# Optimization experiments

Measured on AMD Instinct MI355X. Metric: run time of the kernel, lower is better.

Reference implementation:

```python
import jax, jax.numpy as jnp
import numpy as np

N, C, V, T = 16, 32, 512, 64
H, EMB, D = 4, 64, 16
OUT_C = 64
BN_EPS = 1e-5


def setup_inputs() -> dict:
    key = jax.random.key(0)
    ks = jax.random.split(key, 12)
    x = jax.random.normal(ks[0], (N, C, V, T), dtype=jnp.float32)
    t_in = jax.random.uniform(ks[1], (N, T), dtype=jnp.float32)
    # random-walk-like supports; scaled so chained nconv hops stay O(1)
    A0 = jax.random.normal(ks[2], (V, V), dtype=jnp.float32) * (V ** -0.5)
    A1 = jax.random.normal(ks[3], (V, V), dtype=jnp.float32) * (V ** -0.5)
    A2 = jax.random.normal(ks[4], (V, V), dtype=jnp.float32) * (V ** -0.5)
    factors = jax.random.normal(ks[5], (H,), dtype=jnp.float32) * 0.1
    Wq = jax.random.normal(ks[6], (H, EMB, D), dtype=jnp.float32) * (EMB ** -0.5)
    Wk = jax.random.normal(ks[7], (H, EMB, D), dtype=jnp.float32) * (EMB ** -0.5)
    GC_IN = 7 * C  # (order*support_len + 1) * in_channels
    W_out = jax.random.normal(ks[8], (OUT_C, GC_IN), dtype=jnp.float32) * (GC_IN ** -0.5)
    b_out = jnp.zeros((OUT_C,), dtype=jnp.float32)
    W_res = jax.random.normal(ks[9], (OUT_C, C), dtype=jnp.float32) * (C ** -0.5)
    b_res = jnp.zeros((OUT_C,), dtype=jnp.float32)
    bn_gamma = jnp.ones((OUT_C,), dtype=jnp.float32)
    bn_beta = jnp.zeros((OUT_C,), dtype=jnp.float32)
    bn_mean = jnp.zeros((OUT_C,), dtype=jnp.float32)
    bn_var = jnp.ones((OUT_C,), dtype=jnp.float32)
    alpha = jnp.full((1,), 0.25, dtype=jnp.float32)  # PReLU init
    return dict(x=x, t_in=t_in, A0=A0, A1=A1, A2=A2, factors=factors,
                Wq=Wq, Wk=Wk, W_out=W_out, b_out=b_out,
                W_res=W_res, b_res=b_res, bn_gamma=bn_gamma, bn_beta=bn_beta,
                bn_mean=bn_mean, bn_var=bn_var, alpha=alpha)


def reference(x, t_in, A0, A1, A2, factors, Wq, Wk, W_out, b_out,
              W_res, b_res, bn_gamma, bn_beta, bn_mean, bn_var, alpha):
    # --- learnEmbedding, all heads at once: emb[b,h,t,f] ---
    div = jnp.arange(0, EMB, 2, dtype=x.dtype)           # [EMB/2]
    div_term = jnp.exp(div[None, :] * factors[:, None])  # [H, EMB/2]
    phase = jnp.einsum('bt,hf->bhtf', t_in, div_term)    # [N,H,T,EMB/2]
    emb = jnp.concatenate([jnp.sin(phase), jnp.cos(phase)], axis=-1)  # [N,H,T,EMB]
    # --- ATT per head (t_out=None => q_emb == k_emb) ---
    q = jnp.einsum('bhtf,hfd->bhtd', emb, Wq)
    k = jnp.einsum('bhtf,hfd->bhtd', emb, Wk)
    att = jax.nn.softmax(jnp.einsum('bhtd,bhpd->bhtp', q, k) / (D ** 0.5), axis=-1)  # [N,H,T,T]
    # --- temporal mixing, summed over heads (matches per-head += loop) ---
    xt = jnp.einsum('ncvt,nhpt->ncvp', x, att)           # [N,C,V,T]
    # --- gcn: diffusion over 3 supports, order 2 ---
    outs = [xt]
    for A in (A0, A1, A2):
        x1 = jnp.einsum('ncvl,vw->ncwl', xt, A)
        x2 = jnp.einsum('ncvl,vw->ncwl', x1, A)
        outs.extend([x1, x2])
    h = jnp.concatenate(outs, axis=1)                    # [N,7C,V,T]
    # --- 1x1 output projection ---
    y = jnp.einsum('ncvt,oc->novt', h, W_out) + b_out[None, :, None, None]
    # --- residual branch: 1x1 conv + BatchNorm (eval) ---
    r = jnp.einsum('ncvt,oc->novt', x, W_res) + b_res[None, :, None, None]
    r = (r - bn_mean[None, :, None, None]) * jax.lax.rsqrt(bn_var + BN_EPS)[None, :, None, None]
    r = r * bn_gamma[None, :, None, None] + bn_beta[None, :, None, None]
    # --- residual add + PReLU (dropout is identity in eval) ---
    out = y + r
    out = jnp.where(out > 0, out, alpha[0] * out)
    return out
```

## Files before the change

kernel.cpp:

```cpp
#include <hip/hip_runtime.h>

namespace {
constexpr int N_ = 16, C_ = 32, V_ = 512, T_ = 64;
constexpr int H_ = 4, D_ = 16, OC_ = 64;
constexpr int EMB_ = 64;
constexpr int GCIN_ = 7 * C_;
constexpr int TV_ = T_ * V_;
}

typedef _Float16 f16x8 __attribute__((ext_vector_type(8)));
typedef _Float16 f16x4 __attribute__((ext_vector_type(4)));
typedef float f32x4 __attribute__((ext_vector_type(4)));

__global__ __launch_bounds__(64) void att_kernel(
    const float* __restrict__ t_in, const float* __restrict__ factors,
    const float* __restrict__ Wq, const float* __restrict__ Wk,
    float* __restrict__ att)
{
    const int n = blockIdx.x >> 2;
    const int h = blockIdx.x & 3;
    const int t = threadIdx.x;

    __shared__ float wq_l[EMB_][D_];
    __shared__ float wk_l[EMB_][D_];
    __shared__ float k_l[T_][D_ + 1];

#pragma unroll
    for (int d = 0; d < D_; ++d) {
        wq_l[t][d] = Wq[(h * EMB_ + t) * D_ + d];
        wk_l[t][d] = Wk[(h * EMB_ + t) * D_ + d];
    }
    __syncthreads();

    const float tv = t_in[n * T_ + t];
    const float fh = factors[h];
    float emb[EMB_];
#pragma unroll
    for (int j = 0; j < 32; ++j) {
        float dt = __expf((float)(2 * j) * fh);
        float ph = tv * dt;
        float s, c;
        __sincosf(ph, &s, &c);
        emb[j] = s;
        emb[j + 32] = c;
    }

    float q[D_];
#pragma unroll
    for (int d = 0; d < D_; ++d) {
        float aq = 0.f, ak = 0.f;
#pragma unroll
        for (int f = 0; f < EMB_; ++f) {
            aq += emb[f] * wq_l[f][d];
            ak += emb[f] * wk_l[f][d];
        }
        q[d] = aq;
        k_l[t][d] = ak;
    }
    __syncthreads();

    float L[T_];
    float m = -1e30f;
#pragma unroll
    for (int j = 0; j < T_; ++j) {
        float a = 0.f;
#pragma unroll
        for (int d = 0; d < D_; ++d) a += q[d] * k_l[j][d];
        a *= 0.25f;
        L[j] = a;
        m = fmaxf(m, a);
    }
    float ssum = 0.f;
#pragma unroll
    for (int j = 0; j < T_; ++j) {
        float e = __expf(L[j] - m);
        L[j] = e;
        ssum += e;
    }
    const float inv = 1.f / ssum;
    float* arow = att + (((size_t)(n * H_ + h) * T_ + t) * T_);
#pragma unroll
    for (int j = 0; j < T_; ++j) arow[j] = L[j] * inv;
}

__global__ __launch_bounds__(256) void sred_kernel(
    const float* __restrict__ att, float* __restrict__ S)
{
    int g = blockIdx.x * 256 + threadIdx.x;
    if (g >= N_ * T_ * T_) return;
    int n = g / (T_ * T_);
    int ij = g - n * (T_ * T_);
    float a = 0.f;
#pragma unroll
    for (int h = 0; h < H_; ++h) a += att[(size_t)(n * H_ + h) * (T_ * T_) + ij];
    S[g] = a;
}

__global__ __launch_bounds__(256) void prepAt_kernel(
    const float* __restrict__ A0, const float* __restrict__ A1,
    const float* __restrict__ A2, _Float16* __restrict__ At16)
{
    const int s = blockIdx.z;
    const float* A = (s == 0) ? A0 : ((s == 1) ? A1 : A2);
    const int v0 = blockIdx.y * 32, w0 = blockIdx.x * 32;
    const int tid = threadIdx.x;
    __shared__ float sT[32][33];
#pragma unroll
    for (int k = 0; k < 4; ++k) {
        int lin = k * 256 + tid;
        int i = lin >> 5, w = lin & 31;
        sT[i][w] = A[(size_t)(v0 + i) * V_ + w0 + w];
    }
    __syncthreads();
#pragma unroll
    for (int k = 0; k < 4; ++k) {
        int lin = k * 256 + tid;
        int j = lin >> 5, i = lin & 31;
        At16[(size_t)s * V_ * V_ + (size_t)(w0 + j) * V_ + v0 + i] = (_Float16)sT[i][j];
    }
}

__global__ __launch_bounds__(256) void prepxT_kernel(
    const float* __restrict__ x, _Float16* __restrict__ xT, int n0)
{
    const int b = blockIdx.z;
    const int v0 = blockIdx.x * 32;
    const int t0 = blockIdx.y * 32;
    const int tid = threadIdx.x;
    __shared__ float sT[32][33];
    const float* xb = x + ((size_t)(n0 * C_) + b) * (size_t)(V_ * T_);
    {
        int vi = tid >> 3, tq = tid & 7;
        *(float4*)&sT[vi][tq * 4] = *(const float4*)&xb[(size_t)(v0 + vi) * T_ + t0 + tq * 4];
    }
    __syncthreads();
    {
        int tj = tid >> 3, vq = tid & 7;
        f16x4 o4;
        o4[0] = (_Float16)sT[vq * 4 + 0][tj];
        o4[1] = (_Float16)sT[vq * 4 + 1][tj];
        o4[2] = (_Float16)sT[vq * 4 + 2][tj];
        o4[3] = (_Float16)sT[vq * 4 + 3][tj];
        *(f16x4*)&xT[(size_t)b * TV_ + (size_t)(t0 + tj) * V_ + v0 + vq * 4] = o4;
    }
}

__global__ __launch_bounds__(256) void prepW_kernel(
    const float* __restrict__ W_out, const float* __restrict__ b_out,
    const float* __restrict__ W_res, const float* __restrict__ b_res,
    const float* __restrict__ gamma, const float* __restrict__ beta,
    const float* __restrict__ mean, const float* __restrict__ var,
    _Float16* __restrict__ Wcat, float* __restrict__ bias)
{
    const int tid = threadIdx.x;
    const int o = tid & 63;
    const int kb = tid >> 6;
    const float rs = gamma[o] * rsqrtf(var[o] + 1e-5f);
    for (int kk = 0; kk < 64; ++kk) {
        int k = kb * 64 + kk;
        float w = (k < GCIN_) ? W_out[o * GCIN_ + k] : rs * W_res[o * C_ + (k - GCIN_)];
        Wcat[o * 256 + k] = (_Float16)w;
    }
    if (tid < 64) bias[tid] = b_out[tid] + beta[tid] + rs * (b_res[tid] - mean[tid]);
}

__global__ __launch_bounds__(256) void xtT_kernel(
    const float* __restrict__ x, const float* __restrict__ S,
    _Float16* __restrict__ XT, int n0)
{
    const int b = blockIdx.y;
    const int n = n0 + b / C_;
    const int lane = threadIdx.x & 63;
    const int wav = threadIdx.x >> 6;
    const int vbase = blockIdx.x * 256 + wav * 64;
    const int row16 = lane & 15;
    const int kg = lane >> 4;

    const float* Sn = S + (size_t)n * (T_ * T_);
    const float* xb = x + ((size_t)(n0 * C_) + b) * (V_ * T_);

    f32x4 acc[4][4];
#pragma unroll
    for (int i = 0; i < 4; ++i)
#pragma unroll
        for (int j = 0; j < 4; ++j) acc[i][j] = (f32x4){0.f, 0.f, 0.f, 0.f};

#pragma unroll
    for (int ks = 0; ks < 2; ++ks) {
        f16x8 a[4], bf[4];
#pragma unroll
        for (int mt = 0; mt < 4; ++mt) {
            const float* p = xb + (size_t)(vbase + mt * 16 + row16) * T_ + ks * 32 + kg * 8;
            float4 u = *(const float4*)p;
            float4 w = *(const float4*)(p + 4);
            f16x8 t8;
            t8[0] = (_Float16)u.x; t8[1] = (_Float16)u.y; t8[2] = (_Float16)u.z; t8[3] = (_Float16)u.w;
            t8[4] = (_Float16)w.x; t8[5] = (_Float16)w.y; t8[6] = (_Float16)w.z; t8[7] = (_Float16)w.w;
            a[mt] = t8;
        }
#pragma unroll
        for (int nt = 0; nt < 4; ++nt) {
            const float* p = Sn + (size_t)(nt * 16 + row16) * T_ + ks * 32 + kg * 8;
            float4 u = *(const float4*)p;
            float4 w = *(const float4*)(p + 4);
            f16x8 t8;
            t8[0] = (_Float16)u.x; t8[1] = (_Float16)u.y; t8[2] = (_Float16)u.z; t8[3] = (_Float16)u.w;
            t8[4] = (_Float16)w.x; t8[5] = (_Float16)w.y; t8[6] = (_Float16)w.z; t8[7] = (_Float16)w.w;
            bf[nt] = t8;
        }
#pragma unroll
        for (int nt = 0; nt < 4; ++nt)
#pragma unroll
            for (int mt = 0; mt < 4; ++mt)
                acc[mt][nt] = __builtin_amdgcn_mfma_f32_16x16x32_f16(a[mt], bf[nt], acc[mt][nt], 0, 0, 0);
    }

    _Float16* Yb = XT + (size_t)b * TV_;
#pragma unroll
    for (int mt = 0; mt < 4; ++mt)
#pragma unroll
        for (int nt = 0; nt < 4; ++nt) {
            int p = nt * 16 + row16;
            int v = vbase + mt * 16 + kg * 4;
            f16x4 h;
            h[0] = (_Float16)acc[mt][nt][0];
            h[1] = (_Float16)acc[mt][nt][1];
            h[2] = (_Float16)acc[mt][nt][2];
            h[3] = (_Float16)acc[mt][nt][3];
            *(f16x4*)&Yb[(size_t)p * V_ + v] = h;
        }
}

__global__ __launch_bounds__(512, 4) void hopf_kernel(
    const _Float16* __restrict__ At16, _Float16* __restrict__ Hb,
    unsigned long long ASZ)
{
    const int b = blockIdx.x;
    const int s = blockIdx.y;
    const int tid = threadIdx.x;
    const int lane = tid & 63;
    const int wav = tid >> 6;
    const int wbase = wav * 64;
    const int row16 = lane & 15;
    const int kg = lane >> 4;

    __shared__ _Float16 x1s[T_ * V_];

    const _Float16* At = At16 + (size_t)s * V_ * V_;
    const _Float16* Xb = Hb + (size_t)b * TV_;
    _Float16* Y1 = Hb + (size_t)(1 + 2 * s) * ASZ + (size_t)b * TV_;
    _Float16* Y2 = Hb + (size_t)(2 + 2 * s) * ASZ + (size_t)b * TV_;

    const _Float16* ax = At + (size_t)(wbase + row16) * V_ + kg * 8;
    const _Float16* bx = Xb + (size_t)row16 * V_ + kg * 8;

    f32x4 acc[4][4];
#pragma unroll
    for (int i = 0; i < 4; ++i)
#pragma unroll
        for (int j = 0; j < 4; ++j) acc[i][j] = (f32x4){0.f, 0.f, 0.f, 0.f};

    for (int v0 = 0; v0 < V_; v0 += 32) {
        f16x8 a[4], bf[4];
#pragma unroll
        for (int mt = 0; mt < 4; ++mt)
            a[mt] = *(const f16x8*)(ax + (size_t)mt * 16 * V_ + v0);
#pragma unroll
        for (int nt = 0; nt < 4; ++nt)
            bf[nt] = *(const f16x8*)(bx + (size_t)nt * 16 * V_ + v0);
#pragma unroll
        for (int nt = 0; nt < 4; ++nt)
#pragma unroll
            for (int mt = 0; mt < 4; ++mt)
                acc[mt][nt] = __builtin_amdgcn_mfma_f32_16x16x32_f16(a[mt], bf[nt], acc[mt][nt], 0, 0, 0);
    }

#pragma unroll
    for (int mt = 0; mt < 4; ++mt)
#pragma unroll
        for (int nt = 0; nt < 4; ++nt) {
            int t = nt * 16 + row16;
            int w = wbase + mt * 16 + kg * 4;
            f16x4 h;
            h[0] = (_Float16)acc[mt][nt][0];
            h[1] = (_Float16)acc[mt][nt][1];
            h[2] = (_Float16)acc[mt][nt][2];
            h[3] = (_Float16)acc[mt][nt][3];
            int byte = (t * V_ + w) * 2;
            *(f16x4*)((char*)x1s + (byte ^ ((t & 7) << 4))) = h;
        }
    __syncthreads();

#pragma unroll
    for (int k = 0; k < 8; ++k) {
        int lin = k * 512 + tid;
        int t = lin >> 6;
        int v8 = (lin & 63) << 3;
        int byte = (t * V_ + v8) * 2;
        f16x8 val = *(const f16x8*)((const char*)x1s + (byte ^ ((t & 7) << 4)));
        *(f16x8*)&Y1[(size_t)t * V_ + v8] = val;
    }

#pragma unroll
    for (int i = 0; i < 4; ++i)
#pragma unroll
        for (int j = 0; j < 4; ++j) acc[i][j] = (f32x4){0.f, 0.f, 0.f, 0.f};

    for (int v0 = 0; v0 < V_; v0 += 32) {
        f16x8 a[4], bf[4];
#pragma unroll
        for (int mt = 0; mt < 4; ++mt)
            a[mt] = *(const f16x8*)(ax + (size_t)mt * 16 * V_ + v0);
#pragma unroll
        for (int nt = 0; nt < 4; ++nt) {
            int t = nt * 16 + row16;
            int byte = (t * V_ + v0 + kg * 8) * 2;
            bf[nt] = *(const f16x8*)((const char*)x1s + (byte ^ ((t & 7) << 4)));
        }
#pragma unroll
        for (int nt = 0; nt < 4; ++nt)
#pragma unroll
            for (int mt = 0; mt < 4; ++mt)
                acc[mt][nt] = __builtin_amdgcn_mfma_f32_16x16x32_f16(a[mt], bf[nt], acc[mt][nt], 0, 0, 0);
    }
    __syncthreads();

#pragma unroll
    for (int mt = 0; mt < 4; ++mt)
#pragma unroll
        for (int nt = 0; nt < 4; ++nt) {
            int t = nt * 16 + row16;
            int w = wbase + mt * 16 + kg * 4;
            f16x4 h;
            h[0] = (_Float16)acc[mt][nt][0];
            h[1] = (_Float16)acc[mt][nt][1];
            h[2] = (_Float16)acc[mt][nt][2];
            h[3] = (_Float16)acc[mt][nt][3];
            int byte = (t * V_ + w) * 2;
            *(f16x4*)((char*)x1s + (byte ^ ((t & 7) << 4))) = h;
        }
    __syncthreads();

#pragma unroll
    for (int k = 0; k < 8; ++k) {
        int lin = k * 512 + tid;
        int t = lin >> 6;
        int v8 = (lin & 63) << 3;
        int byte = (t * V_ + v8) * 2;
        f16x8 val = *(const f16x8*)((const char*)x1s + (byte ^ ((t & 7) << 4)));
        *(f16x8*)&Y2[(size_t)t * V_ + v8] = val;
    }
}

__global__ __launch_bounds__(256) void epi_kernel(
    const _Float16* __restrict__ H, unsigned long long ASZ,
    const _Float16* __restrict__ Wcat, const float* __restrict__ bias,
    const float* __restrict__ alpha_p, float* __restrict__ out, int n0)
{
    const int v0 = blockIdx.x * 32;
    const int t0 = blockIdx.y * 8;
    const int nl = blockIdx.z;
    const int ng = n0 + nl;
    const int tid = threadIdx.x;
    const int lane = tid & 63;
    const int wv = tid >> 6;
    const int row16 = lane & 15;
    const int kg = lane >> 4;

    f32x4 acc[2][2][4];
#pragma unroll
    for (int j = 0; j < 2; ++j)
#pragma unroll
        for (int vs = 0; vs < 2; ++vs)
#pragma unroll
            for (int mt = 0; mt < 4; ++mt) acc[j][vs][mt] = (f32x4){0.f, 0.f, 0.f, 0.f};

    const size_t pb = ((size_t)(nl * C_ + kg * 8)) * TV_
                    + (size_t)(t0 + wv * 2) * V_ + v0 + row16;

#pragma unroll
    for (int ks = 0; ks < 8; ++ks) {
        const _Float16* Hk = H + (size_t)ks * ASZ;
        f16x8 a[4];
#pragma unroll
        for (int mt = 0; mt < 4; ++mt)
            a[mt] = *(const f16x8*)(Wcat + (mt * 16 + row16) * 256 + ks * 32 + kg * 8);
#pragma unroll
        for (int j = 0; j < 2; ++j)
#pragma unroll
            for (int vs = 0; vs < 2; ++vs) {
                const _Float16* hp = Hk + pb + (size_t)j * V_ + vs * 16;
                f16x8 bf;
#pragma unroll
                for (int e = 0; e < 8; ++e) bf[e] = hp[(size_t)e * TV_];
#pragma unroll
                for (int mt = 0; mt < 4; ++mt)
                    acc[j][vs][mt] = __builtin_amdgcn_mfma_f32_16x16x32_f16(a[mt], bf, acc[j][vs][mt], 0, 0, 0);
            }
    }

    __shared__ float sC[16 * 33 * 9];
    const float al = alpha_p[0];
    const int ot = tid >> 4;
    const int vvt = tid & 15;

    for (int mt = 0; mt < 4; ++mt) {
#pragma unroll
        for (int j = 0; j < 2; ++j)
#pragma unroll
            for (int vs = 0; vs < 2; ++vs)
#pragma unroll
                for (int r = 0; r < 4; ++r)
                    sC[((kg * 4 + r) * 33 + vs * 16 + row16) * 9 + wv * 2 + j] = acc[j][vs][mt][r];
        __syncthreads();
        const float bo = bias[mt * 16 + ot];
#pragma unroll
        for (int vh = 0; vh < 2; ++vh) {
            const int vl = vvt + vh * 16;
            float vals[8];
#pragma unroll
            for (int tt = 0; tt < 8; ++tt) {
                float u = sC[(ot * 33 + vl) * 9 + tt] + bo;
                vals[tt] = u > 0.f ? u : al * u;
            }
            float* op = out + (((size_t)ng * OC_ + mt * 16 + ot) * V_ + v0 + vl) * T_ + t0;
            *(float4*)&op[0] = make_float4(vals[0], vals[1], vals[2], vals[3]);
            *(float4*)&op[4] = make_float4(vals[4], vals[5], vals[6], vals[7]);
        }
        __syncthreads();
    }
}

extern "C" void kernel_launch(void* const* d_in, const int* in_sizes, int n_in,
                              void* d_out, int out_size, void* d_ws, size_t ws_size,
                              hipStream_t stream)
{
    const float* x       = (const float*)d_in[0];
    const float* t_in    = (const float*)d_in[1];
    const float* A0      = (const float*)d_in[2];
    const float* A1      = (const float*)d_in[3];
    const float* A2      = (const float*)d_in[4];
    const float* factors = (const float*)d_in[5];
    const float* Wq      = (const float*)d_in[6];
    const float* Wk      = (const float*)d_in[7];
    const float* W_out   = (const float*)d_in[8];
    const float* b_out   = (const float*)d_in[9];
    const float* W_res   = (const float*)d_in[10];
    const float* b_res   = (const float*)d_in[11];
    const float* gamma   = (const float*)d_in[12];
    const float* beta    = (const float*)d_in[13];
    const float* mean    = (const float*)d_in[14];
    const float* var     = (const float*)d_in[15];
    const float* alpha   = (const float*)d_in[16];
    float* out = (float*)d_out;

    float* att = (float*)d_ws;
    float* S    = att + (size_t)N_ * H_ * T_ * T_;
    float* bias = S + (size_t)N_ * T_ * T_;
    _Float16* At16 = (_Float16*)(bias + 64);
    _Float16* Wcat = At16 + (size_t)3 * V_ * V_;
    _Float16* Hbase = Wcat + (size_t)64 * 256;

    const size_t fixed = ((size_t)N_ * H_ * T_ * T_ + (size_t)N_ * T_ * T_ + 64) * 4
                       + ((size_t)3 * V_ * V_ + 64 * 256) * 2;
    int Nc = 16;
    while (Nc > 1 && fixed + (size_t)8 * Nc * C_ * T_ * V_ * 2 > ws_size) Nc >>= 1;
    const size_t ASZ = (size_t)Nc * C_ * T_ * V_;

    att_kernel<<<N_ * H_, 64, 0, stream>>>(t_in, factors, Wq, Wk, att);
    sred_kernel<<<(N_ * T_ * T_ + 255) / 256, 256, 0, stream>>>(att, S);
    prepAt_kernel<<<dim3(16, 16, 3), 256, 0, stream>>>(A0, A1, A2, At16);
    prepW_kernel<<<1, 256, 0, stream>>>(W_out, b_out, W_res, b_res,
                                        gamma, beta, mean, var, Wcat, bias);

    for (int n0 = 0; n0 < N_; n0 += Nc) {
        const int nsl = Nc * C_;
        xtT_kernel<<<dim3(2, nsl), 256, 0, stream>>>(x, S, Hbase, n0);
        prepxT_kernel<<<dim3(16, 2, nsl), 256, 0, stream>>>(x, Hbase + (size_t)7 * ASZ, n0);
        hopf_kernel<<<dim3(nsl, 3), 512, 0, stream>>>(At16, Hbase, (unsigned long long)ASZ);
        epi_kernel<<<dim3(16, 8, Nc), 256, 0, stream>>>(
            Hbase, (unsigned long long)ASZ, Wcat, bias, alpha, out, n0);
    }
}
```

Before: 557.3 us.

## Split fused two-hop diffusion into batched GEMM kernels staging A in LDS

Replaces the per-(n,c) fused two-hop kernel, which kept the hop-1 result in shared memory, with a generic hop kernel launched twice. Each block stages a 128x256 slice of the transposed support matrix in swizzled LDS and reuses it across 512 (batch,channel,time) rows, with register double-buffering of the B operand. The aim is to cut repeated global reads of A and raise MFMA reuse, at the cost of writing hop-1 to global memory and reading it back, plus an extra launch.

```diff
diff --git a/kernel.cpp b/kernel.cpp
--- a/kernel.cpp
+++ b/kernel.cpp
@@ -231,125 +231,92 @@
         }
 }
 
-__global__ __launch_bounds__(512, 4) void hopf_kernel(
+__global__ __launch_bounds__(512) void ghop_kernel(
     const _Float16* __restrict__ At16, _Float16* __restrict__ Hb,
-    unsigned long long ASZ)
-{
-    const int b = blockIdx.x;
-    const int s = blockIdx.y;
+    unsigned long long ASZ, int hop)
+{
+    const int btb = blockIdx.x;
+    const int w0 = blockIdx.y * 128;
+    const int s = blockIdx.z;
     const int tid = threadIdx.x;
     const int lane = tid & 63;
     const int wav = tid >> 6;
-    const int wbase = wav * 64;
     const int row16 = lane & 15;
     const int kg = lane >> 4;
 
-    __shared__ _Float16 x1s[T_ * V_];
-
-    const _Float16* At = At16 + (size_t)s * V_ * V_;
-    const _Float16* Xb = Hb + (size_t)b * TV_;
-    _Float16* Y1 = Hb + (size_t)(1 + 2 * s) * ASZ + (size_t)b * TV_;
-    _Float16* Y2 = Hb + (size_t)(2 + 2 * s) * ASZ + (size_t)b * TV_;
-
-    const _Float16* ax = At + (size_t)(wbase + row16) * V_ + kg * 8;
-    const _Float16* bx = Xb + (size_t)row16 * V_ + kg * 8;
-
-    f32x4 acc[4][4];
-#pragma unroll
-    for (int i = 0; i < 4; ++i)
+    __shared__ _Float16 sB[128 * 256];
+
+    const _Float16* Ats = At16 + (size_t)s * V_ * V_;
+    const _Float16* src = Hb + (hop ? (size_t)(1 + 2 * s) * ASZ : 0);
+    _Float16* dst = Hb + (size_t)((hop ? 2 : 1) + 2 * s) * ASZ;
+
+    const size_t btbase = (size_t)btb * 512 + (size_t)wav * 64;
+    const _Float16* bx = src + (btbase + row16) * (size_t)V_;
+
+    f32x4 acc[8][4];
+#pragma unroll
+    for (int i = 0; i < 8; ++i)
 #pragma unroll
         for (int j = 0; j < 4; ++j) acc[i][j] = (f32x4){0.f, 0.f, 0.f, 0.f};
 
-    for (int v0 = 0; v0 < V_; v0 += 32) {
-        f16x8 a[4], bf[4];
-#pragma unroll
-        for (int mt = 0; mt < 4; ++mt)
-            a[mt] = *(const f16x8*)(ax + (size_t)mt * 16 * V_ + v0);
+    const int swr = tid >> 2;
+    const int scq = tid & 3;
+
+    for (int ph = 0; ph < 2; ++ph) {
+        {
+            const _Float16* sp = Ats + (size_t)(w0 + swr) * V_ + ph * 256 + scq * 8;
+#pragma unroll
+            for (int c = 0; c < 8; ++c) {
+                f16x8 val = *(const f16x8*)(sp + c * 32);
+                int byte = (swr * 512 + scq * 16 + c * 64) ^ ((swr & 7) << 4);
+                *(f16x8*)((char*)sB + byte) = val;
+            }
+        }
+        __syncthreads();
+
+        f16x8 bC[4], bN[4];
 #pragma unroll
         for (int nt = 0; nt < 4; ++nt)
-            bf[nt] = *(const f16x8*)(bx + (size_t)nt * 16 * V_ + v0);
-#pragma unroll
-        for (int nt = 0; nt < 4; ++nt)
-#pragma unroll
-            for (int mt = 0; mt < 4; ++mt)
-                acc[mt][nt] = __builtin_amdgcn_mfma_f32_16x16x32_f16(a[mt], bf[nt], acc[mt][nt], 0, 0, 0);
-    }
-
-#pragma unroll
-    for (int mt = 0; mt < 4; ++mt)
+            bC[nt] = *(const f16x8*)(bx + (size_t)nt * 16 * V_ + ph * 256 + kg * 8);
+
+#pragma unroll
+        for (int it = 0; it < 8; ++it) {
+            const int vl = it * 32;
+            if (it < 7) {
+#pragma unroll
+                for (int nt = 0; nt < 4; ++nt)
+                    bN[nt] = *(const f16x8*)(bx + (size_t)nt * 16 * V_ + ph * 256 + vl + 32 + kg * 8);
+            }
+            f16x8 a[8];
+#pragma unroll
+            for (int mt = 0; mt < 8; ++mt) {
+                int byte = ((mt * 16 + row16) * 512 + vl * 2 + kg * 16) ^ ((row16 & 7) << 4);
+                a[mt] = *(const f16x8*)((const char*)sB + byte);
+            }
+#pragma unroll
+            for (int mt = 0; mt < 8; ++mt)
+#pragma unroll
+                for (int nt = 0; nt < 4; ++nt)
+                    acc[mt][nt] = __builtin_amdgcn_mfma_f32_16x16x32_f16(a[mt], bC[nt], acc[mt][nt], 0, 0, 0);
+#pragma unroll
+            for (int nt = 0; nt < 4; ++nt) bC[nt] = bN[nt];
+        }
+        if (ph == 0) __syncthreads();
+    }
+
+#pragma unroll
+    for (int mt = 0; mt < 8; ++mt)
 #pragma unroll
         for (int nt = 0; nt < 4; ++nt) {
-            int t = nt * 16 + row16;
-            int w = wbase + mt * 16 + kg * 4;
+            size_t btr = btbase + nt * 16 + row16;
+            int w = w0 + mt * 16 + kg * 4;
             f16x4 h;
             h[0] = (_Float16)acc[mt][nt][0];
             h[1] = (_Float16)acc[mt][nt][1];
             h[2] = (_Float16)acc[mt][nt][2];
             h[3] = (_Float16)acc[mt][nt][3];
-            int byte = (t * V_ + w) * 2;
-            *(f16x4*)((char*)x1s + (byte ^ ((t & 7) << 4))) = h;
-        }
-    __syncthreads();
-
-#pragma unroll
-    for (int k = 0; k < 8; ++k) {
-        int lin = k * 512 + tid;
-        int t = lin >> 6;
-        int v8 = (lin & 63) << 3;
-        int byte = (t * V_ + v8) * 2;
-        f16x8 val = *(const f16x8*)((const char*)x1s + (byte ^ ((t & 7) << 4)));
-        *(f16x8*)&Y1[(size_t)t * V_ + v8] = val;
-    }
-
-#pragma unroll
-    for (int i = 0; i < 4; ++i)
-#pragma unroll
-        for (int j = 0; j < 4; ++j) acc[i][j] = (f32x4){0.f, 0.f, 0.f, 0.f};
-
-    for (int v0 = 0; v0 < V_; v0 += 32) {
-        f16x8 a[4], bf[4];
-#pragma unroll
-        for (int mt = 0; mt < 4; ++mt)
-            a[mt] = *(const f16x8*)(ax + (size_t)mt * 16 * V_ + v0);
-#pragma unroll
-        for (int nt = 0; nt < 4; ++nt) {
-            int t = nt * 16 + row16;
-            int byte = (t * V_ + v0 + kg * 8) * 2;
-            bf[nt] = *(const f16x8*)((const char*)x1s + (byte ^ ((t & 7) << 4)));
-        }
-#pragma unroll
-        for (int nt = 0; nt < 4; ++nt)
-#pragma unroll
-            for (int mt = 0; mt < 4; ++mt)
-                acc[mt][nt] = __builtin_amdgcn_mfma_f32_16x16x32_f16(a[mt], bf[nt], acc[mt][nt], 0, 0, 0);
-    }
-    __syncthreads();
-
-#pragma unroll
-    for (int mt = 0; mt < 4; ++mt)
-#pragma unroll
-        for (int nt = 0; nt < 4; ++nt) {
-            int t = nt * 16 + row16;
-            int w = wbase + mt * 16 + kg * 4;
-            f16x4 h;
-            h[0] = (_Float16)acc[mt][nt][0];
-            h[1] = (_Float16)acc[mt][nt][1];
-            h[2] = (_Float16)acc[mt][nt][2];
-            h[3] = (_Float16)acc[mt][nt][3];
-            int byte = (t * V_ + w) * 2;
-            *(f16x4*)((char*)x1s + (byte ^ ((t & 7) << 4))) = h;
-        }
-    __syncthreads();
-
-#pragma unroll
-    for (int k = 0; k < 8; ++k) {
-        int lin = k * 512 + tid;
-        int t = lin >> 6;
-        int v8 = (lin & 63) << 3;
-        int byte = (t * V_ + v8) * 2;
-        f16x8 val = *(const f16x8*)((const char*)x1s + (byte ^ ((t & 7) << 4)));
-        *(f16x8*)&Y2[(size_t)t * V_ + v8] = val;
-    }
+            *(f16x4*)&dst[btr * V_ + w] = h;
+        }
 }
 
 __global__ __launch_bounds__(256) void epi_kernel(
@@ -477,7 +444,10 @@
         const int nsl = Nc * C_;
         xtT_kernel<<<dim3(2, nsl), 256, 0, stream>>>(x, S, Hbase, n0);
         prepxT_kernel<<<dim3(16, 2, nsl), 256, 0, stream>>>(x, Hbase + (size_t)7 * ASZ, n0);
-        hopf_kernel<<<dim3(nsl, 3), 512, 0, stream>>>(At16, Hbase, (unsigned long long)ASZ);
+        ghop_kernel<<<dim3(nsl / 8, 4, 3), 512, 0, stream>>>(
+            At16, Hbase, (unsigned long long)ASZ, 0);
+        ghop_kernel<<<dim3(nsl / 8, 4, 3), 512, 0, stream>>>(
+            At16, Hbase, (unsigned long long)ASZ, 1);
         epi_kernel<<<dim3(16, 8, Nc), 256, 0, stream>>>(
             Hbase, (unsigned long long)ASZ, Wcat, bias, alpha, out, n0);
     }
```

New measurement: 690.3 us. 23.9% more time.
